# Optimization experiments

Hardware: AMD Instinct MI355X
Metric: run time of the kernel (lower is better)

## Reference

```python
import jax, jax.numpy as jnp
import numpy as np

B, T, M, K, D = 4, 2048, 16, 16, 128
P = 2 * D          # param_dim = dt_rank(D) + B_rank(D), C_rank=0
E = 2              # expand
DCONV = 2
XPD = (D + P) * E  # 768, conv in-channels
DT_BIAS = 1e-4
LN_EPS = 1e-5


def setup_inputs() -> dict:
    key = jax.random.key(0)
    ks = jax.random.split(key, 8)
    s = lambda i, shape, sc: jax.random.normal(ks[i], shape, jnp.float32) * sc
    return {
        "x": s(0, (B, T, M, D), 1.0),
        "W_in": s(1, (D, XPD + D), 0.02),               # in_proj (no bias), res_dim=D
        "conv_w": s(2, (D + P, XPD, DCONV, 1), 0.02),    # Conv2d OIHW, kernel (d_conv,1)
        "conv_b": jnp.zeros((D + P,), jnp.float32),
        "slots_mu": s(3, (1, K, D), 1.0),                # learnable memory init
        "A_log": jnp.zeros((1,), jnp.float32),           # log(1)=0, A=-exp(A_log)
        "ln_x_g": jnp.ones((D,), jnp.float32),
        "ln_x_b": jnp.zeros((D,), jnp.float32),
        "ln_z_g": jnp.ones((D,), jnp.float32),
        "ln_z_b": jnp.zeros((D,), jnp.float32),
        "Wq": s(4, (D, D), 0.02),
        "Wk": s(5, (D, D), 0.02),
        "Wv": s(6, (D, D), 0.02),
        "Wo": s(7, (D, D), 0.02),
    }


def _ln(x, g, b):
    mu = jnp.mean(x, -1, keepdims=True)
    var = jnp.var(x, -1, keepdims=True)
    return (x - mu) * jax.lax.rsqrt(var + LN_EPS) * g + b


def reference(x, W_in, conv_w, conv_b, slots_mu, A_log,
              ln_x_g, ln_x_b, ln_z_g, ln_z_b, Wq, Wk, Wv, Wo):
    b = x.shape[0]
    # ---- FactsBuildProjection ----
    xp = x @ W_in                                   # [B,T,M,XPD+D]
    xc, res = xp[..., :XPD], xp[..., XPD:]
    res = jax.nn.silu(res)                          # [B,T,M,D] residual gate
    h = jnp.transpose(xc, (0, 3, 1, 2))             # [B,XPD,T,M]
    h = jax.lax.conv_general_dilated(
        h, conv_w, (1, 1), [(DCONV - 1, 0), (0, 0)],  # causal pad along T
        dimension_numbers=("NCHW", "OIHW", "NCHW")) + conv_b[None, :, None, None]
    h = jnp.transpose(h, (0, 2, 3, 1))              # [B,T,M,D+P]
    xs, pe = h[..., :D], h[..., D:]                 # x:[B,T,M,D], pe_params:[B,T,M,P]
    # ---- attention-based slot router (sfmx_attn, 1 head, norm_inputs) ----
    z0 = jnp.broadcast_to(slots_mu, (b, K, D))      # init memory
    xn = _ln(xs, ln_x_g, ln_x_b)
    zn = _ln(z0, ln_z_g, ln_z_b)
    q = zn @ Wq                                     # [B,K,D]
    k = xn @ Wk                                     # [B,T,M,D]
    v = xn @ Wv
    scores = jnp.einsum('bkd,btmd->btkm', q, k) / jnp.sqrt(jnp.float32(D))
    attn = jax.nn.softmax(scores, axis=-1)          # softmax over M inputs
    u = jnp.einsum('btkm,btmd->btkd', attn, v) @ Wo  # routed inputs [B,T,K,D]
    pe_r = jnp.einsum('btkm,btmp->btkp', attn, pe)   # routed params [B,T,K,P]
    # ---- selective scan (diagonal SSM, A scalar rank-1) ----
    dt = jax.nn.softplus(pe_r[..., :D]) + DT_BIAS    # [B,T,K,D]
    Bp = pe_r[..., D:]                               # [B,T,K,D]
    A = -jnp.exp(A_log[0])
    decay = jnp.exp(dt * A)                          # [B,T,K,D]
    dBu = dt * Bp * u                                # [B,T,K,D]

    def step(hprev, inp):
        d, bu = inp
        hn = d * hprev + bu
        return hn, hn

    _, hs = jax.lax.scan(step, z0, (jnp.swapaxes(decay, 0, 1), jnp.swapaxes(dBu, 0, 1)))
    z_all = jnp.swapaxes(hs, 0, 1)                   # [B,T,K,D] memory trajectory
    z_hat = z_all * res                              # residual gate (M==K)
    return z_hat, z_all
```

## Files before the change

### kernel.cpp

```cpp
#include <hip/hip_runtime.h>
#include <cstddef>

#define BN 4
#define TT 2048
#define MM 16
#define KK 16
#define DD 128
#define HO 384
#define RTOT (BN*TT*MM)
#define NTOT ((size_t)BN*TT*KK*DD)
#define LN_EPSf 1e-5f
#define DT_BIASf 1e-4f
#define CHUNKS 64
#define CLEN 32

typedef __attribute__((ext_vector_type(8))) short short8v;
typedef __attribute__((ext_vector_type(4))) float f32x4;

static __device__ __forceinline__ unsigned short f2b(float f) {
    union { float f; unsigned u; } x; x.f = f;
    unsigned r = (x.u + 0x7fffu + ((x.u >> 16) & 1u)) >> 16;
    return (unsigned short)r;
}
static __device__ __forceinline__ uint2 pack4(float a, float b, float c, float d) {
    uint2 r;
    r.x = (unsigned)f2b(a) | ((unsigned)f2b(b) << 16);
    r.y = (unsigned)f2b(c) | ((unsigned)f2b(d) << 16);
    return r;
}
static __device__ __forceinline__ float blo(unsigned u) {
    union { unsigned u; float f; } x; x.u = u << 16; return x.f;
}
static __device__ __forceinline__ float bhi(unsigned u) {
    union { unsigned u; float f; } x; x.u = u & 0xffff0000u; return x.f;
}
static __device__ __forceinline__ void gl_lds16(const void* g, void* l) {
    __builtin_amdgcn_global_load_lds(
        (const __attribute__((address_space(1))) void*)g,
        (__attribute__((address_space(3))) void*)l, 16, 0, 0);
}

__global__ __launch_bounds__(256) void wfold_kernel(const float* __restrict__ W_in,
                                                    const float* __restrict__ conv_w,
                                                    unsigned short* __restrict__ WT) {
    const int n = blockIdx.x, tid = threadIdx.x;
    if (n < HO) {
        __shared__ float cw0[768], cw1[768];
        for (int i = tid; i < 768; i += 256) {
            cw0[i] = conv_w[(n * 768 + i) * 2 + 0];
            cw1[i] = conv_w[(n * 768 + i) * 2 + 1];
        }
        __syncthreads();
        const int k = tid, dd = k & 127;
        const float* cw = (k < 128) ? cw0 : cw1;
        const float* wr = W_in + (size_t)dd * 896;
        float acc = 0.f;
        #pragma unroll 8
        for (int i = 0; i < 768; ++i) acc += wr[i] * cw[i];
        WT[(size_t)n * 256 + k] = f2b(acc);
    } else {
        const int k = tid;
        float v = (k < 128) ? 0.f : W_in[(size_t)(k - 128) * 896 + 768 + (n - HO)];
        WT[(size_t)n * 256 + k] = f2b(v);
    }
}

__global__ __launch_bounds__(128) void w3_kernel(const float* __restrict__ slots_mu,
                                                 const float* __restrict__ ln_z_g,
                                                 const float* __restrict__ ln_z_b,
                                                 const float* __restrict__ Wq,
                                                 const float* __restrict__ Wk,
                                                 const float* __restrict__ Wv,
                                                 const float* __restrict__ Wo,
                                                 unsigned short* __restrict__ W3T) {
    const int n = blockIdx.x, tid = threadIdx.x;
    if (n < 128) {
        __shared__ float wo[128];
        wo[tid] = Wo[(size_t)tid * 128 + n];
        __syncthreads();
        const float* wv = Wv + (size_t)tid * 128;
        float acc = 0.f;
        #pragma unroll 8
        for (int c = 0; c < 128; ++c) acc += wv[c] * wo[c];
        W3T[(size_t)n * 128 + tid] = f2b(acc);
    } else {
        const int k2 = n - 128;
        __shared__ float zn[128], qv[128];
        __shared__ float red[4];
        float v = slots_mu[(size_t)k2 * 128 + tid];
        float s = v, ss = v * v;
        #pragma unroll
        for (int o = 32; o; o >>= 1) { s += __shfl_xor(s, o); ss += __shfl_xor(ss, o); }
        if ((tid & 63) == 0) { red[(tid >> 6) * 2] = s; red[(tid >> 6) * 2 + 1] = ss; }
        __syncthreads();
        float S = red[0] + red[2], SS = red[1] + red[3];
        float mu = S * (1.f / 128.f), var = SS * (1.f / 128.f) - mu * mu;
        float rs = rsqrtf(var + LN_EPSf);
        zn[tid] = (v - mu) * rs * ln_z_g[tid] + ln_z_b[tid];
        __syncthreads();
        float a = 0.f;
        for (int dd2 = 0; dd2 < 128; ++dd2) a += zn[dd2] * Wq[(size_t)dd2 * 128 + tid];
        qv[tid] = a;
        __syncthreads();
        float qp = 0.f;
        for (int c = 0; c < 128; ++c) qp += qv[c] * Wk[(size_t)tid * 128 + c];
        W3T[(size_t)n * 128 + tid] = f2b(qp * 0.08838834764831845f);
    }
}

__global__ __launch_bounds__(256) void cvt_kernel(const float* __restrict__ x,
                                                  unsigned short* __restrict__ Xb,
                                                  float* __restrict__ zbuf) {
    if (blockIdx.x == 0 && threadIdx.x < 64) zbuf[threadIdx.x] = 0.f;
    const size_t t0 = (size_t)blockIdx.x * 256 + threadIdx.x;
    #pragma unroll
    for (int it = 0; it < 4; ++it) {
        size_t i = t0 + (size_t)it * 1048576;
        float4 v = ((const float4*)x)[i];
        union { unsigned short s[4]; unsigned long long ll; } o;
        o.s[0] = f2b(v.x); o.s[1] = f2b(v.y); o.s[2] = f2b(v.z); o.s[3] = f2b(v.w);
        ((unsigned long long*)Xb)[i] = o.ll;
    }
}

__global__ __launch_bounds__(256) void gemm1_kernel(const unsigned short* __restrict__ Xb,
                                                    const unsigned short* __restrict__ WT,
                                                    const float* __restrict__ zbuf,
                                                    const float* __restrict__ conv_b,
                                                    const float* __restrict__ ln_x_g,
                                                    const float* __restrict__ ln_x_b,
                                                    unsigned short* __restrict__ xnB,
                                                    unsigned short* __restrict__ Hpe,
                                                    float* __restrict__ resg) {
    __shared__ unsigned short Asm[128 * 64];
    __shared__ unsigned short Bsm[128 * 64];

    const int bid = blockIdx.x;
    const int ct = bid & 3, rt = bid >> 2;
    const int tid = threadIdx.x;
    const int wv = tid >> 6, l = tid & 63;
    const int lr = l & 15, g = l >> 4;
    const int rowbase = rt * 128;
    const int colbase = ct * 128;

    const int srow = (wv * 8) + (l >> 3);
    const char* XbB = (const char*)Xb;
    const char* WTB = (const char*)WT;
    char* AsmB = (char*)Asm;
    char* BsmB = (char*)Bsm;

    f32x4 acc[2][8];
    #pragma unroll
    for (int i = 0; i < 2; ++i)
        #pragma unroll
        for (int j = 0; j < 8; ++j) acc[i][j] = (f32x4)0.f;

    const bool edge = (rt & 255) == 0;

    #pragma unroll
    for (int ks = 0; ks < 4; ++ks) {
        #pragma unroll
        for (int j = 0; j < 4; ++j) {
            const int seg = wv * 4 + j;
            const int row = seg * 8 + (l >> 3);
            const int chunk = l & 7;
            const int gch = chunk ^ (row & 7);
            {
                const int grow = rowbase + row + (ks < 2 ? -16 : 0);
                const bool ok = (ks >= 2) || !edge || (row >= 16);
                const char* src = ok ? (XbB + ((size_t)grow * 256 + (ks & 1) * 128 + gch * 16))
                                     : (const char*)zbuf;
                gl_lds16(src, AsmB + seg * 1024);
            }
            {
                const int n = colbase + row;
                gl_lds16(WTB + ((size_t)n * 512 + ks * 128 + gch * 16), BsmB + seg * 1024);
            }
        }
        __syncthreads();

        #pragma unroll
        for (int kb = 0; kb < 2; ++kb) {
            short8v a[2], b[8];
            #pragma unroll
            for (int mf = 0; mf < 2; ++mf) {
                const int arow = wv * 32 + mf * 16 + lr;
                const int aoff = arow * 128 + (((kb * 4 + g) ^ (arow & 7)) * 16);
                a[mf] = *(const short8v*)(AsmB + aoff);
            }
            #pragma unroll
            for (int nf = 0; nf < 8; ++nf) {
                const int brow = nf * 16 + lr;
                const int boff = brow * 128 + (((kb * 4 + g) ^ (brow & 7)) * 16);
                b[nf] = *(const short8v*)(BsmB + boff);
            }
            #pragma unroll
            for (int mf = 0; mf < 2; ++mf)
                #pragma unroll
                for (int nf = 0; nf < 8; ++nf)
                    acc[mf][nf] = __builtin_amdgcn_mfma_f32_16x16x32_bf16(b[nf], a[mf], acc[mf][nf], 0, 0, 0);
        }
        __syncthreads();
    }

    if (ct == 0) {
        f32x4 cb[8];
        #pragma unroll
        for (int nf = 0; nf < 8; ++nf) cb[nf] = *(const f32x4*)(conv_b + nf * 16 + g * 4);
        #pragma unroll
        for (int mf = 0; mf < 2; ++mf) {
            float s = 0.f, ss = 0.f;
            #pragma unroll
            for (int nf = 0; nf < 8; ++nf)
                #pragma unroll
                for (int r = 0; r < 4; ++r) {
                    float v = acc[mf][nf][r] + cb[nf][r];
                    acc[mf][nf][r] = v;
                    s += v; ss += v * v;
                }
            s += __shfl_xor(s, 16);  s += __shfl_xor(s, 32);
            ss += __shfl_xor(ss, 16); ss += __shfl_xor(ss, 32);
            float mu = s * (1.f / 128.f);
            float var = ss * (1.f / 128.f) - mu * mu;
            float rs = rsqrtf(var + LN_EPSf);
            const int row = rowbase + wv * 32 + mf * 16 + lr;
            #pragma unroll
            for (int nf = 0; nf < 8; ++nf) {
                f32x4 gv = *(const f32x4*)(ln_x_g + nf * 16 + g * 4);
                f32x4 bv = *(const f32x4*)(ln_x_b + nf * 16 + g * 4);
                float o0 = (acc[mf][nf][0] - mu) * rs * gv[0] + bv[0];
                float o1 = (acc[mf][nf][1] - mu) * rs * gv[1] + bv[1];
                float o2 = (acc[mf][nf][2] - mu) * rs * gv[2] + bv[2];
                float o3 = (acc[mf][nf][3] - mu) * rs * gv[3] + bv[3];
                *(uint2*)(xnB + (size_t)row * DD + nf * 16 + g * 4) = pack4(o0, o1, o2, o3);
            }
        }
    } else if (ct < 3) {
        #pragma unroll
        for (int mf = 0; mf < 2; ++mf) {
            const int row = rowbase + wv * 32 + mf * 16 + lr;
            #pragma unroll
            for (int nf = 0; nf < 8; ++nf) {
                const int col = colbase + nf * 16 + g * 4;
                f32x4 cb = *(const f32x4*)(conv_b + col);
                *(uint2*)(Hpe + (size_t)row * 256 + (col - 128)) =
                    pack4(acc[mf][nf][0] + cb[0], acc[mf][nf][1] + cb[1],
                          acc[mf][nf][2] + cb[2], acc[mf][nf][3] + cb[3]);
            }
        }
    } else {
        #pragma unroll
        for (int mf = 0; mf < 2; ++mf) {
            const int row = rowbase + wv * 32 + mf * 16 + lr;
            #pragma unroll
            for (int nf = 0; nf < 8; ++nf) {
                f32x4 o;
                #pragma unroll
                for (int r = 0; r < 4; ++r) {
                    float v = acc[mf][nf][r];
                    o[r] = v / (1.f + expf(-v));
                }
                *(f32x4*)(resg + (size_t)row * DD + nf * 16 + g * 4) = o;
            }
        }
    }
}

__global__ __launch_bounds__(256) void gemm3f_kernel(const unsigned short* __restrict__ xnB,
                                                     const unsigned short* __restrict__ W3T,
                                                     const unsigned short* __restrict__ Hpe,
                                                     const float* __restrict__ A_log,
                                                     float* __restrict__ decayg,
                                                     float* __restrict__ dBug) {
    __shared__ float sV[4][16 * 130 + 2];
    __shared__ float sA[4][256];
    const int tid = threadIdx.x, wv = tid >> 6, l = tid & 63;
    const int lr = l & 15, g = l >> 4, lk = g * 8;
    const int bt = blockIdx.x * 4 + wv;
    const int rb = bt * 16;

    f32x4 acc[9];
    #pragma unroll
    for (int j = 0; j < 9; ++j) acc[j] = (f32x4)0.f;

    #pragma unroll
    for (int ks = 0; ks < 4; ++ks) {
        short8v a = *(const short8v*)(xnB + (size_t)(rb + lr) * DD + ks * 32 + lk);
        #pragma unroll
        for (int nf = 0; nf < 9; ++nf) {
            short8v b = *(const short8v*)(W3T + (size_t)(nf * 16 + lr) * DD + ks * 32 + lk);
            acc[nf] = __builtin_amdgcn_mfma_f32_16x16x32_bf16(b, a, acc[nf], 0, 0, 0);
        }
    }

    #pragma unroll
    for (int r = 0; r < 4; ++r) {
        float sc = acc[8][r];
        float mx = sc;
        #pragma unroll
        for (int off = 1; off <= 8; off <<= 1) mx = fmaxf(mx, __shfl_xor(mx, off));
        float p = expf(sc - mx);
        float sm = p;
        #pragma unroll
        for (int off = 1; off <= 8; off <<= 1) sm += __shfl_xor(sm, off);
        sA[wv][lr * 16 + g * 4 + r] = p / sm;
    }
    #pragma unroll
    for (int nf = 0; nf < 8; ++nf) {
        float* dst = &sV[wv][lr * 130 + nf * 16 + g * 4];
        *(float2*)dst = make_float2(acc[nf][0], acc[nf][1]);
        *(float2*)(dst + 2) = make_float2(acc[nf][2], acc[nf][3]);
    }
    __syncthreads();

    float vo0[16], vo1[16];
    unsigned pe0[16], pe1[16];
    #pragma unroll
    for (int m = 0; m < 16; ++m) {
        float2 t = *(const float2*)&sV[wv][m * 130 + 2 * l];
        vo0[m] = t.x; vo1[m] = t.y;
        pe0[m] = *(const unsigned*)(Hpe + (size_t)(rb + m) * 256 + 2 * l);
        pe1[m] = *(const unsigned*)(Hpe + (size_t)(rb + m) * 256 + 128 + 2 * l);
    }
    const float A = -expf(A_log[0]);
    for (int k2 = 0; k2 < 16; ++k2) {
        float u0 = 0.f, u1 = 0.f, pd0 = 0.f, pd1 = 0.f, pb0 = 0.f, pb1 = 0.f;
        #pragma unroll
        for (int m = 0; m < 16; ++m) {
            float a = sA[wv][m * 16 + k2];
            u0 += a * vo0[m];       u1 += a * vo1[m];
            pd0 += a * blo(pe0[m]); pd1 += a * bhi(pe0[m]);
            pb0 += a * blo(pe1[m]); pb1 += a * bhi(pe1[m]);
        }
        float dt0 = fmaxf(pd0, 0.f) + log1pf(expf(-fabsf(pd0))) + DT_BIASf;
        float dt1 = fmaxf(pd1, 0.f) + log1pf(expf(-fabsf(pd1))) + DT_BIASf;
        float de0 = expf(dt0 * A), de1 = expf(dt1 * A);
        float db0 = dt0 * pb0 * u0, db1 = dt1 * pb1 * u1;
        size_t o = ((size_t)bt * KK + k2) * DD + 2 * l;
        *(float2*)(decayg + o) = make_float2(de0, de1);
        *(float2*)(dBug + o)   = make_float2(db0, db1);
    }
}

__global__ __launch_bounds__(128) void scanA_kernel(const float* decayg, const float* dBug,
                                                    float* __restrict__ Pc, float* __restrict__ Sc) {
    const int c = blockIdx.x & (CHUNKS - 1), bk = blockIdx.x >> 6;
    const int b = bk >> 4, k2 = bk & 15, d = threadIdx.x;
    const size_t base = (((size_t)b * TT + c * CLEN) * KK + k2) * DD + d;
    float P = 1.f, S = 0.f;
    #pragma unroll 4
    for (int j = 0; j < CLEN; ++j) {
        size_t idx = base + (size_t)j * (KK * DD);
        float de = decayg[idx], db = dBug[idx];
        P *= de;
        S = fmaf(de, S, db);
    }
    Pc[(size_t)blockIdx.x * DD + d] = P;
    Sc[(size_t)blockIdx.x * DD + d] = S;
}

__global__ __launch_bounds__(128) void scanB_kernel(const float* __restrict__ Pc,
                                                    const float* __restrict__ Sc,
                                                    const float* __restrict__ slots_mu,
                                                    float* __restrict__ Hinit) {
    const int bk = blockIdx.x, k2 = bk & 15, d = threadIdx.x;
    float h = slots_mu[(size_t)k2 * DD + d];
    #pragma unroll 8
    for (int c = 0; c < CHUNKS; ++c) {
        size_t i = ((size_t)bk * CHUNKS + c) * DD + d;
        Hinit[i] = h;
        h = fmaf(Pc[i], h, Sc[i]);
    }
}

__global__ __launch_bounds__(128) void scanC_kernel(const float* decayg, const float* dBug,
                                                    const float* __restrict__ resg,
                                                    const float* __restrict__ Hinit,
                                                    float* outA, float* outB) {
    const int c = blockIdx.x & (CHUNKS - 1), bk = blockIdx.x >> 6;
    const int b = bk >> 4, k2 = bk & 15, d = threadIdx.x;
    const size_t base = (((size_t)b * TT + c * CLEN) * KK + k2) * DD + d;
    float h = Hinit[((size_t)bk * CHUNKS + c) * DD + d];
    #pragma unroll 4
    for (int j = 0; j < CLEN; ++j) {
        size_t idx = base + (size_t)j * (KK * DD);
        float de = decayg[idx], db = dBug[idx];
        h = fmaf(de, h, db);
        outA[idx] = h * resg[idx];
        outB[idx] = h;
    }
}

extern "C" void kernel_launch(void* const* d_in, const int* in_sizes, int n_in,
                              void* d_out, int out_size, void* d_ws, size_t ws_size,
                              hipStream_t stream) {
    const float* x        = (const float*)d_in[0];
    const float* W_in     = (const float*)d_in[1];
    const float* conv_w   = (const float*)d_in[2];
    const float* conv_b   = (const float*)d_in[3];
    const float* slots_mu = (const float*)d_in[4];
    const float* A_log    = (const float*)d_in[5];
    const float* ln_x_g   = (const float*)d_in[6];
    const float* ln_x_b   = (const float*)d_in[7];
    const float* ln_z_g   = (const float*)d_in[8];
    const float* ln_z_b   = (const float*)d_in[9];
    const float* Wq       = (const float*)d_in[10];
    const float* Wk       = (const float*)d_in[11];
    const float* Wv       = (const float*)d_in[12];
    const float* Wo       = (const float*)d_in[13];

    char* w = (char*)d_ws;
    auto give = [&](size_t bytes) -> char* {
        char* r = w; w += (bytes + 255) & ~(size_t)255; return r;
    };
    float* zbuf = (float*)give(256);
    unsigned short* WT  = (unsigned short*)give((size_t)512 * 256 * 2);
    unsigned short* W3T = (unsigned short*)give((size_t)144 * 128 * 2);
    unsigned short* Xb  = (unsigned short*)give((size_t)RTOT * 128 * 2);
    unsigned short* xnB = (unsigned short*)give((size_t)RTOT * 128 * 2);
    unsigned short* Hpe = (unsigned short*)give((size_t)RTOT * 256 * 2);
    float* resg  = (float*)give((size_t)RTOT * 128 * 4);
    float* Pc    = (float*)give((size_t)4096 * 128 * 4);
    float* Sc    = (float*)give((size_t)4096 * 128 * 4);
    float* Hinit = (float*)give((size_t)64 * CHUNKS * 128 * 4);

    float* decayg = (float*)d_out;
    float* dBug   = ((float*)d_out) + NTOT;

    wfold_kernel<<<dim3(512), dim3(256), 0, stream>>>(W_in, conv_w, WT);
    w3_kernel<<<dim3(144), dim3(128), 0, stream>>>(slots_mu, ln_z_g, ln_z_b, Wq, Wk, Wv, Wo, W3T);
    cvt_kernel<<<dim3(4096), dim3(256), 0, stream>>>(x, Xb, zbuf);
    gemm1_kernel<<<dim3(4096), dim3(256), 0, stream>>>(Xb, WT, zbuf, conv_b, ln_x_g, ln_x_b, xnB, Hpe, resg);
    gemm3f_kernel<<<dim3(2048), dim3(256), 0, stream>>>(xnB, W3T, Hpe, A_log, decayg, dBug);
    scanA_kernel<<<dim3(4096), dim3(128), 0, stream>>>(decayg, dBug, Pc, Sc);
    scanB_kernel<<<dim3(64), dim3(128), 0, stream>>>(Pc, Sc, slots_mu, Hinit);
    scanC_kernel<<<dim3(4096), dim3(128), 0, stream>>>(decayg, dBug, resg, Hinit, decayg, dBug);
}
```

Measured before the change: 503.1 us.

## Route attention-weighted sums through MFMA with transposed pe layout

The scalar per-slot routing loops in gemm3f (attn·V and attn·pe, through shared memory) become bf16 MFMA ops. Attention probabilities and V are packed into MFMA operands with lane shuffles. gemm1 now writes the pe parameters in a per-(b,t) transposed layout so they load directly as MFMA B fragments. Softmax and softplus switch to fast __expf/__logf intrinsics. This removes LDS staging and a syncthreads, but rounds attention and V to bf16 and makes the pe stores scattered 2-byte writes.

```diff
diff --git a/kernel.cpp b/kernel.cpp
--- a/kernel.cpp
+++ b/kernel.cpp
@@ -22,17 +22,16 @@
     unsigned r = (x.u + 0x7fffu + ((x.u >> 16) & 1u)) >> 16;
     return (unsigned short)r;
 }
+static __device__ __forceinline__ unsigned pk2(float a, float b) {
+    return (unsigned)f2b(a) | ((unsigned)f2b(b) << 16);
+}
 static __device__ __forceinline__ uint2 pack4(float a, float b, float c, float d) {
-    uint2 r;
-    r.x = (unsigned)f2b(a) | ((unsigned)f2b(b) << 16);
-    r.y = (unsigned)f2b(c) | ((unsigned)f2b(d) << 16);
-    return r;
-}
-static __device__ __forceinline__ float blo(unsigned u) {
-    union { unsigned u; float f; } x; x.u = u << 16; return x.f;
-}
-static __device__ __forceinline__ float bhi(unsigned u) {
-    union { unsigned u; float f; } x; x.u = u & 0xffff0000u; return x.f;
+    uint2 r; r.x = pk2(a, b); r.y = pk2(c, d); return r;
+}
+static __device__ __forceinline__ short8v mk8(unsigned a, unsigned b, unsigned c, unsigned d) {
+    union { unsigned u[4]; short8v v; } x;
+    x.u[0] = a; x.u[1] = b; x.u[2] = c; x.u[3] = d;
+    return x.v;
 }
 static __device__ __forceinline__ void gl_lds16(const void* g, void* l) {
     __builtin_amdgcn_global_load_lds(
@@ -130,7 +129,7 @@
                                                     const float* __restrict__ ln_x_g,
                                                     const float* __restrict__ ln_x_b,
                                                     unsigned short* __restrict__ xnB,
-                                                    unsigned short* __restrict__ Hpe,
+                                                    unsigned short* __restrict__ peT,
                                                     float* __restrict__ resg) {
     __shared__ unsigned short Asm[128 * 64];
     __shared__ unsigned short Bsm[128 * 64];
@@ -143,7 +142,6 @@
     const int rowbase = rt * 128;
     const int colbase = ct * 128;
 
-    const int srow = (wv * 8) + (l >> 3);
     const char* XbB = (const char*)Xb;
     const char* WTB = (const char*)WT;
     char* AsmB = (char*)Asm;
@@ -236,16 +234,20 @@
             }
         }
     } else if (ct < 3) {
+        f32x4 cb[8];
+        #pragma unroll
+        for (int nf = 0; nf < 8; ++nf) cb[nf] = *(const f32x4*)(conv_b + colbase + nf * 16 + g * 4);
         #pragma unroll
         for (int mf = 0; mf < 2; ++mf) {
-            const int row = rowbase + wv * 32 + mf * 16 + lr;
+            const int btq = rt * 8 + wv * 2 + mf;
+            unsigned short* dst = peT + (size_t)btq * 4096 + lr;
+            const int pbase = (colbase - 128) + g * 4;
             #pragma unroll
             for (int nf = 0; nf < 8; ++nf) {
-                const int col = colbase + nf * 16 + g * 4;
-                f32x4 cb = *(const f32x4*)(conv_b + col);
-                *(uint2*)(Hpe + (size_t)row * 256 + (col - 128)) =
-                    pack4(acc[mf][nf][0] + cb[0], acc[mf][nf][1] + cb[1],
-                          acc[mf][nf][2] + cb[2], acc[mf][nf][3] + cb[3]);
+                #pragma unroll
+                for (int r = 0; r < 4; ++r) {
+                    dst[(size_t)(pbase + nf * 16 + r) * 16] = f2b(acc[mf][nf][r] + cb[nf][r]);
+                }
             }
         }
     } else {
@@ -258,7 +260,7 @@
                 #pragma unroll
                 for (int r = 0; r < 4; ++r) {
                     float v = acc[mf][nf][r];
-                    o[r] = v / (1.f + expf(-v));
+                    o[r] = v / (1.f + __expf(-v));
                 }
                 *(f32x4*)(resg + (size_t)row * DD + nf * 16 + g * 4) = o;
             }
@@ -268,77 +270,78 @@
 
 __global__ __launch_bounds__(256) void gemm3f_kernel(const unsigned short* __restrict__ xnB,
                                                      const unsigned short* __restrict__ W3T,
-                                                     const unsigned short* __restrict__ Hpe,
+                                                     const unsigned short* __restrict__ peT,
                                                      const float* __restrict__ A_log,
                                                      float* __restrict__ decayg,
                                                      float* __restrict__ dBug) {
-    __shared__ float sV[4][16 * 130 + 2];
-    __shared__ float sA[4][256];
     const int tid = threadIdx.x, wv = tid >> 6, l = tid & 63;
-    const int lr = l & 15, g = l >> 4, lk = g * 8;
+    const int lr = l & 15, g = l >> 4;
     const int bt = blockIdx.x * 4 + wv;
     const int rb = bt * 16;
 
     f32x4 acc[9];
     #pragma unroll
     for (int j = 0; j < 9; ++j) acc[j] = (f32x4)0.f;
-
     #pragma unroll
     for (int ks = 0; ks < 4; ++ks) {
-        short8v a = *(const short8v*)(xnB + (size_t)(rb + lr) * DD + ks * 32 + lk);
+        short8v a = *(const short8v*)(xnB + (size_t)(rb + lr) * DD + ks * 32 + g * 8);
         #pragma unroll
         for (int nf = 0; nf < 9; ++nf) {
-            short8v b = *(const short8v*)(W3T + (size_t)(nf * 16 + lr) * DD + ks * 32 + lk);
-            acc[nf] = __builtin_amdgcn_mfma_f32_16x16x32_bf16(b, a, acc[nf], 0, 0, 0);
-        }
-    }
-
-    #pragma unroll
-    for (int r = 0; r < 4; ++r) {
-        float sc = acc[8][r];
-        float mx = sc;
-        #pragma unroll
-        for (int off = 1; off <= 8; off <<= 1) mx = fmaxf(mx, __shfl_xor(mx, off));
-        float p = expf(sc - mx);
-        float sm = p;
-        #pragma unroll
-        for (int off = 1; off <= 8; off <<= 1) sm += __shfl_xor(sm, off);
-        sA[wv][lr * 16 + g * 4 + r] = p / sm;
-    }
+            short8v b = *(const short8v*)(W3T + (size_t)(nf * 16 + lr) * DD + ks * 32 + g * 8);
+            acc[nf] = __builtin_amdgcn_mfma_f32_16x16x32_bf16(a, b, acc[nf], 0, 0, 0);
+        }
+    }
+
+    float mx = fmaxf(fmaxf(acc[8][0], acc[8][1]), fmaxf(acc[8][2], acc[8][3]));
+    mx = fmaxf(mx, __shfl_xor(mx, 16));
+    mx = fmaxf(mx, __shfl_xor(mx, 32));
+    float p0 = __expf(acc[8][0] - mx), p1 = __expf(acc[8][1] - mx);
+    float p2 = __expf(acc[8][2] - mx), p3 = __expf(acc[8][3] - mx);
+    float sm = p0 + p1 + p2 + p3;
+    sm += __shfl_xor(sm, 16);
+    sm += __shfl_xor(sm, 32);
+    const float inv = 1.f / sm;
+
+    const int srcA = lr + ((g & 1) << 5), srcB = srcA + 16;
+    unsigned PA0 = pk2(p0 * inv, p1 * inv);
+    unsigned PA1 = pk2(p2 * inv, p3 * inv);
+    unsigned A0 = __shfl(PA0, srcA), A1 = __shfl(PA1, srcA);
+    unsigned A2 = __shfl(PA0, srcB), A3 = __shfl(PA1, srcB);
+    if (g >= 2) { A0 = 0; A1 = 0; A2 = 0; A3 = 0; }
+    const short8v attnA = mk8(A0, A1, A2, A3);
+
+    f32x4 pvo[8];
     #pragma unroll
     for (int nf = 0; nf < 8; ++nf) {
-        float* dst = &sV[wv][lr * 130 + nf * 16 + g * 4];
-        *(float2*)dst = make_float2(acc[nf][0], acc[nf][1]);
-        *(float2*)(dst + 2) = make_float2(acc[nf][2], acc[nf][3]);
-    }
-    __syncthreads();
-
-    float vo0[16], vo1[16];
-    unsigned pe0[16], pe1[16];
-    #pragma unroll
-    for (int m = 0; m < 16; ++m) {
-        float2 t = *(const float2*)&sV[wv][m * 130 + 2 * l];
-        vo0[m] = t.x; vo1[m] = t.y;
-        pe0[m] = *(const unsigned*)(Hpe + (size_t)(rb + m) * 256 + 2 * l);
-        pe1[m] = *(const unsigned*)(Hpe + (size_t)(rb + m) * 256 + 128 + 2 * l);
-    }
-    const float A = -expf(A_log[0]);
-    for (int k2 = 0; k2 < 16; ++k2) {
-        float u0 = 0.f, u1 = 0.f, pd0 = 0.f, pd1 = 0.f, pb0 = 0.f, pb1 = 0.f;
-        #pragma unroll
-        for (int m = 0; m < 16; ++m) {
-            float a = sA[wv][m * 16 + k2];
-            u0 += a * vo0[m];       u1 += a * vo1[m];
-            pd0 += a * blo(pe0[m]); pd1 += a * bhi(pe0[m]);
-            pb0 += a * blo(pe1[m]); pb1 += a * bhi(pe1[m]);
-        }
-        float dt0 = fmaxf(pd0, 0.f) + log1pf(expf(-fabsf(pd0))) + DT_BIASf;
-        float dt1 = fmaxf(pd1, 0.f) + log1pf(expf(-fabsf(pd1))) + DT_BIASf;
-        float de0 = expf(dt0 * A), de1 = expf(dt1 * A);
-        float db0 = dt0 * pb0 * u0, db1 = dt1 * pb1 * u1;
-        size_t o = ((size_t)bt * KK + k2) * DD + 2 * l;
-        *(float2*)(decayg + o) = make_float2(de0, de1);
-        *(float2*)(dBug + o)   = make_float2(db0, db1);
+        unsigned Q0 = pk2(acc[nf][0], acc[nf][1]);
+        unsigned Q1 = pk2(acc[nf][2], acc[nf][3]);
+        short8v bf = mk8(__shfl(Q0, srcA), __shfl(Q1, srcA), __shfl(Q0, srcB), __shfl(Q1, srcB));
+        pvo[nf] = __builtin_amdgcn_mfma_f32_16x16x32_bf16(attnA, bf, (f32x4)0.f, 0, 0, 0);
+    }
+
+    f32x4 ppe[16];
+    const unsigned short* pbase = peT + (size_t)bt * 4096 + g * 8;
+    #pragma unroll
+    for (int nf = 0; nf < 16; ++nf) {
+        short8v bf = *(const short8v*)(pbase + (nf * 16 + lr) * 16);
+        ppe[nf] = __builtin_amdgcn_mfma_f32_16x16x32_bf16(attnA, bf, (f32x4)0.f, 0, 0, 0);
+    }
+
+    const float A = -__expf(A_log[0]);
+    #pragma unroll
+    for (int nf = 0; nf < 8; ++nf) {
+        const int d = nf * 16 + lr;
+        #pragma unroll
+        for (int r = 0; r < 4; ++r) {
+            const int k2 = g * 4 + r;
+            float pd = ppe[nf][r];
+            float pb = ppe[nf + 8][r];
+            float u  = pvo[nf][r];
+            float dt = fmaxf(pd, 0.f) + __logf(1.f + __expf(-fabsf(pd))) + DT_BIASf;
+            size_t o = (size_t)bt * 2048 + (size_t)k2 * 128 + d;
+            decayg[o] = __expf(dt * A);
+            dBug[o]   = dt * pb * u;
+        }
     }
 }
 
@@ -418,7 +421,7 @@
     unsigned short* W3T = (unsigned short*)give((size_t)144 * 128 * 2);
     unsigned short* Xb  = (unsigned short*)give((size_t)RTOT * 128 * 2);
     unsigned short* xnB = (unsigned short*)give((size_t)RTOT * 128 * 2);
-    unsigned short* Hpe = (unsigned short*)give((size_t)RTOT * 256 * 2);
+    unsigned short* peT = (unsigned short*)give((size_t)RTOT * 256 * 2 + 256);
     float* resg  = (float*)give((size_t)RTOT * 128 * 4);
     float* Pc    = (float*)give((size_t)4096 * 128 * 4);
     float* Sc    = (float*)give((size_t)4096 * 128 * 4);
@@ -430,8 +433,8 @@
     wfold_kernel<<<dim3(512), dim3(256), 0, stream>>>(W_in, conv_w, WT);
     w3_kernel<<<dim3(144), dim3(128), 0, stream>>>(slots_mu, ln_z_g, ln_z_b, Wq, Wk, Wv, Wo, W3T);
     cvt_kernel<<<dim3(4096), dim3(256), 0, stream>>>(x, Xb, zbuf);
-    gemm1_kernel<<<dim3(4096), dim3(256), 0, stream>>>(Xb, WT, zbuf, conv_b, ln_x_g, ln_x_b, xnB, Hpe, resg);
-    gemm3f_kernel<<<dim3(2048), dim3(256), 0, stream>>>(xnB, W3T, Hpe, A_log, decayg, dBug);
+    gemm1_kernel<<<dim3(4096), dim3(256), 0, stream>>>(Xb, WT, zbuf, conv_b, ln_x_g, ln_x_b, xnB, peT, resg);
+    gemm3f_kernel<<<dim3(2048), dim3(256), 0, stream>>>(xnB, W3T, peT, A_log, decayg, dBug);
     scanA_kernel<<<dim3(4096), dim3(128), 0, stream>>>(decayg, dBug, Pc, Sc);
     scanB_kernel<<<dim3(64), dim3(128), 0, stream>>>(Pc, Sc, slots_mu, Hinit);
     scanC_kernel<<<dim3(4096), dim3(128), 0, stream>>>(decayg, dBug, resg, Hinit, decayg, dBug);
```

Result: faster. 467.7 us (-7.0%).
